# Kernel tuning notes

Hardware: AMD Instinct MI355X
Metric: run time of the kernel (lower is better)

The kernel has to match this reference:

```python
import jax, jax.numpy as jnp
import numpy as np

NUM_HEADS = 8


def setup_inputs() -> dict:
    key = jax.random.key(0)
    ks = jax.random.split(key, 7)
    B, D, N = 16, 512, 2048
    sc = 1.0 / np.sqrt(D)
    return {
        "X_Query": jax.random.normal(ks[0], (B, D, N), jnp.float32),
        "X_Key": jax.random.normal(ks[1], (B, D, N), jnp.float32),
        "X_Value": jax.random.normal(ks[2], (B, D, N), jnp.float32),
        "W_q": jax.random.normal(ks[3], (D, D), jnp.float32) * sc,
        "W_k": jax.random.normal(ks[4], (D, D), jnp.float32) * sc,
        "W_v": jax.random.normal(ks[5], (D, D), jnp.float32) * sc,
        "W_o": jax.random.normal(ks[6], (D, D), jnp.float32) * sc,
    }


def _proj(W, x):
    # Conv1d(D, D, kernel_size=1, bias=False) == channel matmul
    return jnp.einsum('oi,bin->bon', W, x)


def _split_heads(x, h):
    # torch: cat(x.chunk(h, dim=-1), dim=0) -> (h, B, D, N/h) stacked layout
    B, D, N = x.shape
    return x.reshape(B, D, h, N // h).transpose(2, 0, 1, 3)


def _mha(XQ, XK, XV, Wq, Wk, Wv, Wo):
    B, D, N = XQ.shape
    h = NUM_HEADS
    Nh = N // h
    q = _split_heads(_proj(Wq, XQ), h)  # (h, B, D, Nh)
    k = _split_heads(_proj(Wk, XK), h)
    v = _split_heads(_proj(Wv, XV), h)
    # scores over the CHANNEL axis: (h, B, D, D), scaled by sqrt(d_k)=sqrt(Nh)
    scores = jnp.einsum('hbdn,hben->hbde', q, k) / jnp.sqrt(jnp.asarray(Nh, q.dtype))
    p = jax.nn.softmax(scores, axis=-1)
    out = jnp.einsum('hbde,hben->hbdn', p, v)  # (h, B, D, Nh)
    # torch: cat(chunks, dim=0) inverse -> cat along dim=-1
    attn_heads = out.transpose(1, 2, 0, 3).reshape(B, D, N)
    return _proj(Wo, XQ - attn_heads)


def reference(X_Query, X_Key, X_Value, W_q, W_k, W_v, W_o):
    return _mha(X_Query, X_Key, X_Value, W_q, W_k, W_v, W_o)
```

## Files before the change

kernel.cpp:

```cpp
#include <hip/hip_runtime.h>
#include <hip/hip_bf16.h>

#define DD  512
#define NN  2048
#define BB  16
#define NHD 256

typedef unsigned short u16;
typedef __attribute__((ext_vector_type(4))) float f32x4;
typedef __attribute__((ext_vector_type(8))) short s16x8;
typedef __attribute__((ext_vector_type(4))) short s16x4;
typedef __attribute__((ext_vector_type(4))) u16   u16x4;

static __device__ __forceinline__ u16 f2bf(float f) {
  __hip_bfloat16 h = __float2bfloat16(f);
  return *reinterpret_cast<u16*>(&h);
}
static __device__ __forceinline__ float bf2f(u16 u) {
  union { unsigned int i; float f; } v; v.i = ((unsigned int)u) << 16; return v.f;
}
static __device__ __forceinline__ f32x4 mfma_bf16(s16x8 a, s16x8 b, f32x4 c) {
  return __builtin_amdgcn_mfma_f32_16x16x32_bf16(a, b, c, 0, 0, 0);
}
static __device__ __forceinline__ void gload_lds16(const u16* g, u16* l) {
  __builtin_amdgcn_global_load_lds(
      (const __attribute__((address_space(1))) unsigned int*)g,
      (__attribute__((address_space(3))) unsigned int*)l, 16, 0, 0);
}
static __device__ __forceinline__ void barrier_raw() {
  __builtin_amdgcn_sched_barrier(0);
  __builtin_amdgcn_s_barrier();
  __builtin_amdgcn_sched_barrier(0);
}
#define WAITCNT(s) do { asm volatile("s_waitcnt " s ::: "memory"); \
                        __builtin_amdgcn_sched_barrier(0); } while (0)

__global__ __launch_bounds__(256) void k_cvt_w(const float* __restrict__ w0,
                                               const float* __restrict__ w1,
                                               const float* __restrict__ w2,
                                               const float* __restrict__ w3,
                                               u16* __restrict__ out) {
  const float* srcs[4] = {w0, w1, w2, w3};
  const float* s = srcs[blockIdx.y];
  u16* o = out + (size_t)blockIdx.y * (DD * DD);
  int idx = blockIdx.x * 256 + threadIdx.x;
  float4 v = *(const float4*)(s + (size_t)idx * 4);
  u16x4 u = {f2bf(v.x), f2bf(v.y), f2bf(v.z), f2bf(v.w)};
  *(u16x4*)(o + (size_t)idx * 4) = u;
}

template <bool XA>
__global__ __launch_bounds__(256) void k_gemm_proj(
    const float* __restrict__ X, const u16* __restrict__ W,
    u16* __restrict__ C, long long c_bs, int ldc) {
  __shared__ __align__(16) u16 Xb[2][128 * 64];
  __shared__ __align__(16) u16 Wt[2][128 * 64];
  const int tid = threadIdx.x;
  const int lane = tid & 63, w = tid >> 6;
  const int wm = (w >> 1) * 64, wn = (w & 1) * 64;
  const int r = lane & 15, g = lane >> 4;
  f32x4 acc[4][4] = {};

  const int m0 = blockIdx.x * 128, n0 = blockIdx.y * 128, b = blockIdx.z;
  const int xbase = XA ? m0 : n0;
  const int wbase = XA ? n0 : m0;
  const float* Xg = X + (size_t)b * DD * NN + xbase;
  const u16* Wg = W + (size_t)wbase * DD;

  const int nq = tid & 31, ib = (tid >> 5) * 4;
  float4 rv[8];
  auto issue_x = [&](int kt) {
#pragma unroll
    for (int j = 0; j < 2; ++j)
#pragma unroll
      for (int ii = 0; ii < 4; ++ii)
        rv[j * 4 + ii] =
            *(const float4*)(Xg + (size_t)(kt * 64 + j * 32 + ib + ii) * NN + nq * 4);
  };
  auto stage_w = [&](int buf, int kt) {
#pragma unroll
    for (int j2 = 0; j2 < 4; ++j2) {
      int s = j2 * 256 + tid;
      int row = s >> 3, u = s & 7;
      gload_lds16(Wg + (size_t)row * DD + kt * 64 + ((u ^ (row & 7)) * 8),
                  &Wt[buf][s * 8]);
    }
  };
  auto write_x = [&](int buf) {
#pragma unroll
    for (int j = 0; j < 2; ++j) {
      const int k0 = j * 32 + ib;
      const float4 a0 = rv[j*4], a1 = rv[j*4+1], a2 = rv[j*4+2], a3 = rv[j*4+3];
#pragma unroll
      for (int e = 0; e < 4; ++e) {
        const int row = nq * 4 + e;
        float v0, v1, v2, v3;
        if      (e == 0) { v0=a0.x; v1=a1.x; v2=a2.x; v3=a3.x; }
        else if (e == 1) { v0=a0.y; v1=a1.y; v2=a2.y; v3=a3.y; }
        else if (e == 2) { v0=a0.z; v1=a1.z; v2=a2.z; v3=a3.z; }
        else             { v0=a0.w; v1=a1.w; v2=a2.w; v3=a3.w; }
        u16x4 pk = {f2bf(v0), f2bf(v1), f2bf(v2), f2bf(v3)};
        *(u16x4*)((char*)&Xb[buf][0] + row * 128 +
                  (((k0 >> 3) ^ (row & 7)) * 16) + (k0 & 7) * 2) = pk;
      }
    }
  };

  issue_x(0); stage_w(0, 0);
  for (int kt = 0; kt < 8; ++kt) {
    WAITCNT("vmcnt(0)");
    barrier_raw();
    write_x(kt & 1);
    if (kt < 7) { issue_x(kt + 1); stage_w((kt + 1) & 1, kt + 1); }
    WAITCNT("lgkmcnt(0)");
    barrier_raw();
    {
      const u16* Ab_ = XA ? &Xb[kt & 1][0] : &Wt[kt & 1][0];
      const u16* Bb_ = XA ? &Wt[kt & 1][0] : &Xb[kt & 1][0];
#pragma unroll
      for (int ks = 0; ks < 2; ++ks) {
        s16x8 av[4], bv[4];
#pragma unroll
        for (int m = 0; m < 4; ++m) {
          int row = wm + m * 16 + r;
          av[m] = *(const s16x8*)&Ab_[row * 64 + (((ks * 4 + g) ^ (row & 7)) * 8)];
        }
#pragma unroll
        for (int nf = 0; nf < 4; ++nf) {
          int row = wn + nf * 16 + r;
          bv[nf] = *(const s16x8*)&Bb_[row * 64 + (((ks * 4 + g) ^ (row & 7)) * 8)];
        }
#pragma unroll
        for (int m = 0; m < 4; ++m)
#pragma unroll
          for (int nf = 0; nf < 4; ++nf)
            acc[m][nf] = mfma_bf16(av[m], bv[nf], acc[m][nf]);
      }
    }
    WAITCNT("lgkmcnt(0)");
  }

  u16* Cg = C + (size_t)b * c_bs;
#pragma unroll
  for (int m = 0; m < 4; ++m)
#pragma unroll
    for (int nf = 0; nf < 4; ++nf)
#pragma unroll
      for (int j = 0; j < 4; ++j) {
        int row = m0 + wm + m * 16 + g * 4 + j;
        int col = n0 + wn + nf * 16 + r;
        Cg[(size_t)row * ldc + col] = f2bf(acc[m][nf][j]);
      }
}

#define GEMM_STAGE(Ag, lda, Bg, ldb, buf, kt)                                   \
  {                                                                             \
    _Pragma("unroll")                                                           \
    for (int j = 0; j < 4; ++j) {                                               \
      int s = j * 256 + w * 64 + lane;                                          \
      int row = s >> 3, u = s & 7;                                              \
      int col = ((u ^ (row & 7)) * 8);                                          \
      gload_lds16(Ag + (size_t)row * lda + (kt) * 64 + col, &Ab[buf][s * 8]);   \
      gload_lds16(Bg + (size_t)row * ldb + (kt) * 64 + col, &Bb[buf][s * 8]);   \
    }                                                                           \
  }

#define GEMM_COMPUTE(buf)                                                       \
  {                                                                             \
    _Pragma("unroll")                                                           \
    for (int ks = 0; ks < 2; ++ks) {                                            \
      s16x8 av[4], bv[4];                                                       \
      _Pragma("unroll")                                                         \
      for (int m = 0; m < 4; ++m) {                                             \
        int row = wm + m * 16 + r;                                              \
        av[m] = *(const s16x8*)&Ab[buf][row * 64 + (((ks * 4 + g) ^ (row & 7)) * 8)]; \
      }                                                                         \
      _Pragma("unroll")                                                         \
      for (int nf = 0; nf < 4; ++nf) {                                          \
        int row = wn + nf * 16 + r;                                             \
        bv[nf] = *(const s16x8*)&Bb[buf][row * 64 + (((ks * 4 + g) ^ (row & 7)) * 8)]; \
      }                                                                         \
      _Pragma("unroll")                                                         \
      for (int m = 0; m < 4; ++m)                                               \
        _Pragma("unroll")                                                       \
        for (int nf = 0; nf < 4; ++nf)                                          \
          acc[m][nf] = mfma_bf16(av[m], bv[nf], acc[m][nf]);                    \
    }                                                                           \
  }

#define GEMM_PREAMBLE                                                           \
  __shared__ __align__(16) u16 Ab[2][128 * 64];                                 \
  __shared__ __align__(16) u16 Bb[2][128 * 64];                                 \
  const int tid = threadIdx.x;                                                  \
  const int lane = tid & 63, w = tid >> 6;                                      \
  const int wm = (w >> 1) * 64, wn = (w & 1) * 64;                              \
  const int r = lane & 15, g = lane >> 4;                                       \
  f32x4 acc[4][4] = {};

#define GEMM_MAINLOOP(Ag, lda, Bg, ldb, nkt)                                    \
  GEMM_STAGE(Ag, lda, Bg, ldb, 0, 0);                                           \
  __syncthreads();                                                              \
  for (int kt = 0; kt < (nkt) - 1; ++kt) {                                      \
    GEMM_STAGE(Ag, lda, Bg, ldb, (kt & 1) ^ 1, kt + 1);                         \
    GEMM_COMPUTE(kt & 1);                                                       \
    __syncthreads();                                                            \
  }                                                                             \
  GEMM_COMPUTE(((nkt) - 1) & 1);

template <typename OUT_T>
__global__ __launch_bounds__(256) void k_gemm_nt(
    const u16* __restrict__ A, long long a_bs, int lda,
    const u16* __restrict__ B, long long b_bs, int ldb,
    OUT_T* __restrict__ C, long long c_bs, int ldc, int K) {
  GEMM_PREAMBLE
  const int m0 = blockIdx.x * 128, n0 = blockIdx.y * 128;
  const u16* Ag = A + (size_t)blockIdx.z * a_bs + (size_t)m0 * lda;
  const u16* Bg = B + (size_t)blockIdx.z * b_bs + (size_t)n0 * ldb;
  const int nkt = K >> 6;
  GEMM_MAINLOOP(Ag, lda, Bg, ldb, nkt);

  OUT_T* Cg = C + (size_t)blockIdx.z * c_bs;
#pragma unroll
  for (int m = 0; m < 4; ++m)
#pragma unroll
    for (int nf = 0; nf < 4; ++nf)
#pragma unroll
      for (int j = 0; j < 4; ++j) {
        int row = m0 + wm + m * 16 + g * 4 + j;
        int col = n0 + wn + nf * 16 + r;
        float v = acc[m][nf][j];
        if constexpr (sizeof(OUT_T) == 2) Cg[(size_t)row * ldc + col] = f2bf(v);
        else                              Cg[(size_t)row * ldc + col] = v;
      }
}

__global__ __launch_bounds__(512, 4) void k_attn_fused(
    const u16* __restrict__ Qdn, const u16* __restrict__ Kdn,
    const u16* __restrict__ VT,  const float* __restrict__ Xq,
    u16* __restrict__ And) {
  __shared__ __align__(16) u16 L[35072];
  u16* Kr = L;
  u16* Vr = L + 16384;
  u16* Ps = L + 32768;

  const int tid = threadIdx.x;
  const int lane = tid & 63, w = tid >> 6;
  const int r = lane & 15, g = lane >> 4;
  const int dq = w >> 1, eh = w & 1;
  const int nq = w >> 1, dh = w & 1;
  const int bid = blockIdx.x;
  const int dt = bid >> 7, hb = bid & 127;
  const int h = hb & 7, b = hb >> 3;
  const int d0 = dt * 64, hn0 = h * NHD;

  const u16* Qg = Qdn + ((size_t)b * DD + d0) * NN + hn0;
  const u16* Kg = Kdn + ((size_t)b * DD) * NN + hn0;
  const u16* Vg = VT + ((size_t)b * NN + hn0) * DD;

  auto stage_ket = [&](int et) {
    u16* dst = Kr + (et & 1) * 8192;
    const u16* src = Kg + (size_t)(et * 32) * NN;
#pragma unroll
    for (int j = 0; j < 2; ++j) {
      int s = j * 512 + tid;
      int row = s >> 5, u = s & 31;
      gload_lds16(src + (size_t)row * NN + ((u ^ (row & 7)) * 8), dst + s * 8);
    }
  };
  auto stage_vet = [&](int et) {
    u16* dst = Vr + (et & 1) * 8192;
    int rl = tid >> 2, u = tid & 3;
#pragma unroll
    for (int j = 0; j < 2; ++j) {
      int gn = (rl >> 5) * 64 + j * 32 + (rl & 31);
      gload_lds16(Vg + (size_t)gn * DD + et * 32 + ((u ^ (rl & 3)) * 8),
                  dst + j * 4096 + tid * 8);
    }
  };

#pragma unroll
  for (int jj = 0; jj < 4; ++jj) {
    int s = jj * 512 + tid;
    int row = s >> 5, u = s & 31;
    gload_lds16(Qg + (size_t)row * NN + ((u ^ (row & 7)) * 8), L + s * 8);
  }
  WAITCNT("vmcnt(0)");
  barrier_raw();
  s16x8 qf[8];
  {
    const int qrow = dq * 16 + r;
#pragma unroll
    for (int k2 = 0; k2 < 8; ++k2)
      qf[k2] = *(const s16x8*)&L[qrow * 256 + (((k2 * 4 + g) ^ (qrow & 7)) * 8)];
  }
  WAITCNT("lgkmcnt(0)");
  barrier_raw();
  stage_ket(0); stage_vet(0);

  float psum[4] = {};
  f32x4 acc_o[2][2][2] = {};

  for (int et = 0; et < 16; ++et) {
    WAITCNT("vmcnt(2)");
    barrier_raw();
    f32x4 acc_s = {};
    const u16* kb = Kr + (et & 1) * 8192;
    const int rowe = eh * 16 + r;
    __builtin_amdgcn_s_setprio(1);
#pragma unroll
    for (int kq = 0; kq < 8; ++kq) {
      s16x8 bv = *(const s16x8*)&kb[rowe * 256 + (((kq * 4 + g) ^ (rowe & 7)) * 8)];
      acc_s = mfma_bf16(qf[kq], bv, acc_s);
    }
    __builtin_amdgcn_s_setprio(0);
    WAITCNT("lgkmcnt(0)");
    barrier_raw();
    if (et + 1 < 16) { stage_ket(et + 1); stage_vet(et + 1); }
#pragma unroll
    for (int j = 0; j < 4; ++j) {
      int rowd = dq * 16 + g * 4 + j;
      int cole = eh * 16 + r;
      float p = __expf(acc_s[j] * 0.0625f);
      psum[j] += p;
      Ps[rowd * 36 + cole] = f2bf(p);
    }
    WAITCNT("lgkmcnt(0)");
    if (et < 15) WAITCNT("vmcnt(4)");
    else         WAITCNT("vmcnt(0)");
    barrier_raw();
    s16x8 pb[2];
#pragma unroll
    for (int nf = 0; nf < 2; ++nf) {
      int rowd = dh * 32 + nf * 16 + r;
      s16x4 plo = *(const s16x4*)&Ps[rowd * 36 + g * 8];
      s16x4 phi = *(const s16x4*)&Ps[rowd * 36 + g * 8 + 4];
      pb[nf] = __builtin_shufflevector(plo, phi, 0, 1, 2, 3, 4, 5, 6, 7);
    }
    __builtin_amdgcn_s_setprio(1);
#pragma unroll
    for (int j = 0; j < 2; ++j) {
      const u16* vb = Vr + (et & 1) * 8192 + j * 4096;
#pragma unroll
      for (int ms = 0; ms < 2; ++ms) {
        int rl = nq * 32 + ms * 16 + r;
        s16x8 av = *(const s16x8*)((const char*)vb + rl * 64 + ((g * 16) ^ ((rl & 3) << 4)));
        acc_o[j][ms][0] = mfma_bf16(av, pb[0], acc_o[j][ms][0]);
        acc_o[j][ms][1] = mfma_bf16(av, pb[1], acc_o[j][ms][1]);
      }
    }
    __builtin_amdgcn_s_setprio(0);
    WAITCNT("lgkmcnt(0)");
  }

  barrier_raw();
  float* rs = (float*)L;
#pragma unroll
  for (int j = 0; j < 4; ++j) {
    float v = psum[j];
    v += __shfl_xor(v, 1);
    v += __shfl_xor(v, 2);
    v += __shfl_xor(v, 4);
    v += __shfl_xor(v, 8);
    if (r == 0) rs[w * 16 + g * 4 + j] = v;
  }
  __syncthreads();
  if (tid < 64) {
    int dqi = tid >> 4, i = tid & 15;
    rs[128 + tid] = 1.0f / (rs[(dqi * 2) * 16 + i] + rs[(dqi * 2 + 1) * 16 + i]);
  }
  __syncthreads();

  const float* Xqf = Xq + ((size_t)b * DD + d0) * NN + hn0;
  u16* Ag = And + ((size_t)b * NN + hn0) * DD + d0;
#pragma unroll
  for (int j = 0; j < 2; ++j)
#pragma unroll
    for (int ms = 0; ms < 2; ++ms)
#pragma unroll
      for (int nf = 0; nf < 2; ++nf) {
        const int dc = dh * 32 + nf * 16 + r;
        const float inv = rs[128 + dc];
#pragma unroll
        for (int jj = 0; jj < 4; ++jj) {
          const int npos = nq * 64 + j * 32 + ms * 16 + g * 4 + jj;
          float o = acc_o[j][ms][nf][jj] * inv;
          float xq = Xqf[(size_t)dc * NN + npos];
          Ag[(size_t)npos * DD + dc] = f2bf(xq - o);
        }
      }
}

extern "C" void kernel_launch(void* const* d_in, const int* in_sizes, int n_in,
                              void* d_out, int out_size, void* d_ws, size_t ws_size,
                              hipStream_t stream) {
  const float* Xq = (const float*)d_in[0];
  const float* Xk = (const float*)d_in[1];
  const float* Xv = (const float*)d_in[2];
  const float* Wq = (const float*)d_in[3];
  const float* Wk = (const float*)d_in[4];
  const float* Wv = (const float*)d_in[5];
  const float* Wo = (const float*)d_in[6];
  float* out = (float*)d_out;

  char* ws = (char*)d_ws;
  const size_t MB = 1024 * 1024;
  u16* Wb  = (u16*)ws;
  u16* Qdn = (u16*)(ws + 2 * MB);
  u16* And = (u16*)(ws + 34 * MB);
  u16* VTb = (u16*)d_out;
  u16* Kdn = (u16*)d_out + (size_t)BB * NN * DD;

  k_cvt_w<<<dim3(256, 4), 256, 0, stream>>>(Wq, Wk, Wv, Wo, Wb);

  k_gemm_proj<false><<<dim3(DD / 128, NN / 128, BB), 256, 0, stream>>>(
      Xq, Wb, Qdn, (long long)DD * NN, NN);
  k_gemm_proj<false><<<dim3(DD / 128, NN / 128, BB), 256, 0, stream>>>(
      Xk, Wb + DD * DD, Kdn, (long long)DD * NN, NN);
  k_gemm_proj<true><<<dim3(NN / 128, DD / 128, BB), 256, 0, stream>>>(
      Xv, Wb + 2 * DD * DD, VTb, (long long)NN * DD, DD);

  k_attn_fused<<<dim3(1024), 512, 0, stream>>>(Qdn, Kdn, VTb, Xq, And);

  k_gemm_nt<float><<<dim3(DD / 128, NN / 128, BB), 256, 0, stream>>>(
      Wb + 3 * DD * DD, 0, DD,
      And, (long long)NN * DD, DD,
      out, (long long)DD * NN, NN, DD);
}
```

Baseline: 256.5 us.

## Read projection weights directly from global memory and stage Xq tile through LDS

The projection GEMM stops staging weight tiles into shared memory. MFMA operands for the weights now come straight from global memory (expected to hit in L2/L1), and the X tile uses a single LDS buffer with a reworked transpose-write pattern. This frees LDS and removes the W staging loads, but it drops double buffering and adds a barrier per k-step. Separately, the attention epilogue first loads the Xq tile into LDS with coalesced float4 loads, so the residual subtraction no longer does strided scalar global reads.

```diff
diff --git a/kernel.cpp b/kernel.cpp
--- a/kernel.cpp
+++ b/kernel.cpp
@@ -53,8 +53,7 @@
 __global__ __launch_bounds__(256) void k_gemm_proj(
     const float* __restrict__ X, const u16* __restrict__ W,
     u16* __restrict__ C, long long c_bs, int ldc) {
-  __shared__ __align__(16) u16 Xb[2][128 * 64];
-  __shared__ __align__(16) u16 Wt[2][128 * 64];
+  __shared__ __align__(16) u16 Xb[128 * 64];
   const int tid = threadIdx.x;
   const int lane = tid & 63, w = tid >> 6;
   const int wm = (w >> 1) * 64, wn = (w & 1) * 64;
@@ -62,82 +61,63 @@
   f32x4 acc[4][4] = {};
 
   const int m0 = blockIdx.x * 128, n0 = blockIdx.y * 128, b = blockIdx.z;
-  const int xbase = XA ? m0 : n0;
-  const int wbase = XA ? n0 : m0;
-  const float* Xg = X + (size_t)b * DD * NN + xbase;
-  const u16* Wg = W + (size_t)wbase * DD;
-
-  const int nq = tid & 31, ib = (tid >> 5) * 4;
+  const int nb = XA ? m0 : n0;
+  const int wb = XA ? n0 : m0;
+  const float* Xg = X + (size_t)b * DD * NN + nb;
+  const u16* Wg = W + (size_t)wb * DD;
+
+  const int n4 = (tid & 31) * 4;
+  const int k8 = (tid >> 5) * 8;
   float4 rv[8];
   auto issue_x = [&](int kt) {
 #pragma unroll
-    for (int j = 0; j < 2; ++j)
-#pragma unroll
-      for (int ii = 0; ii < 4; ++ii)
-        rv[j * 4 + ii] =
-            *(const float4*)(Xg + (size_t)(kt * 64 + j * 32 + ib + ii) * NN + nq * 4);
+    for (int kk = 0; kk < 8; ++kk)
+      rv[kk] = *(const float4*)(Xg + (size_t)(kt * 64 + k8 + kk) * NN + n4);
   };
-  auto stage_w = [&](int buf, int kt) {
-#pragma unroll
-    for (int j2 = 0; j2 < 4; ++j2) {
-      int s = j2 * 256 + tid;
-      int row = s >> 3, u = s & 7;
-      gload_lds16(Wg + (size_t)row * DD + kt * 64 + ((u ^ (row & 7)) * 8),
-                  &Wt[buf][s * 8]);
+  auto write_x = [&]() {
+#pragma unroll
+    for (int e = 0; e < 4; ++e) {
+      const int row = n4 + e;
+      const int base = row * 128 + (((k8 >> 3) ^ (row & 7)) * 16);
+#pragma unroll
+      for (int kb = 0; kb < 2; ++kb) {
+        u16x4 pk = {f2bf(rv[kb * 4 + 0][e]), f2bf(rv[kb * 4 + 1][e]),
+                    f2bf(rv[kb * 4 + 2][e]), f2bf(rv[kb * 4 + 3][e])};
+        *(u16x4*)((char*)Xb + base + kb * 8) = pk;
+      }
     }
   };
-  auto write_x = [&](int buf) {
-#pragma unroll
-    for (int j = 0; j < 2; ++j) {
-      const int k0 = j * 32 + ib;
-      const float4 a0 = rv[j*4], a1 = rv[j*4+1], a2 = rv[j*4+2], a3 = rv[j*4+3];
-#pragma unroll
-      for (int e = 0; e < 4; ++e) {
-        const int row = nq * 4 + e;
-        float v0, v1, v2, v3;
-        if      (e == 0) { v0=a0.x; v1=a1.x; v2=a2.x; v3=a3.x; }
-        else if (e == 1) { v0=a0.y; v1=a1.y; v2=a2.y; v3=a3.y; }
-        else if (e == 2) { v0=a0.z; v1=a1.z; v2=a2.z; v3=a3.z; }
-        else             { v0=a0.w; v1=a1.w; v2=a2.w; v3=a3.w; }
-        u16x4 pk = {f2bf(v0), f2bf(v1), f2bf(v2), f2bf(v3)};
-        *(u16x4*)((char*)&Xb[buf][0] + row * 128 +
-                  (((k0 >> 3) ^ (row & 7)) * 16) + (k0 & 7) * 2) = pk;
-      }
-    }
-  };
-
-  issue_x(0); stage_w(0, 0);
+
+  issue_x(0);
   for (int kt = 0; kt < 8; ++kt) {
     WAITCNT("vmcnt(0)");
-    barrier_raw();
-    write_x(kt & 1);
-    if (kt < 7) { issue_x(kt + 1); stage_w((kt + 1) & 1, kt + 1); }
+    write_x();
+    if (kt < 7) issue_x(kt + 1);
     WAITCNT("lgkmcnt(0)");
     barrier_raw();
-    {
-      const u16* Ab_ = XA ? &Xb[kt & 1][0] : &Wt[kt & 1][0];
-      const u16* Bb_ = XA ? &Wt[kt & 1][0] : &Xb[kt & 1][0];
-#pragma unroll
-      for (int ks = 0; ks < 2; ++ks) {
-        s16x8 av[4], bv[4];
-#pragma unroll
-        for (int m = 0; m < 4; ++m) {
-          int row = wm + m * 16 + r;
-          av[m] = *(const s16x8*)&Ab_[row * 64 + (((ks * 4 + g) ^ (row & 7)) * 8)];
-        }
-#pragma unroll
-        for (int nf = 0; nf < 4; ++nf) {
-          int row = wn + nf * 16 + r;
-          bv[nf] = *(const s16x8*)&Bb_[row * 64 + (((ks * 4 + g) ^ (row & 7)) * 8)];
-        }
-#pragma unroll
-        for (int m = 0; m < 4; ++m)
-#pragma unroll
-          for (int nf = 0; nf < 4; ++nf)
-            acc[m][nf] = mfma_bf16(av[m], bv[nf], acc[m][nf]);
-      }
+#pragma unroll
+    for (int ks = 0; ks < 2; ++ks) {
+      s16x8 wv[4], xv[4];
+#pragma unroll
+      for (int m = 0; m < 4; ++m) {
+        int wrow = (XA ? wn : wm) + m * 16 + r;
+        wv[m] = *(const s16x8*)(Wg + (size_t)wrow * DD + kt * 64 + (ks * 4 + g) * 8);
+      }
+#pragma unroll
+      for (int m = 0; m < 4; ++m) {
+        int xrow = (XA ? wm : wn) + m * 16 + r;
+        xv[m] = *(const s16x8*)((char*)Xb + xrow * 128 +
+                                (((ks * 4 + g) ^ (xrow & 7)) * 16));
+      }
+#pragma unroll
+      for (int m = 0; m < 4; ++m)
+#pragma unroll
+        for (int nf = 0; nf < 4; ++nf)
+          acc[m][nf] = XA ? mfma_bf16(xv[m], wv[nf], acc[m][nf])
+                          : mfma_bf16(wv[m], xv[nf], acc[m][nf]);
     }
     WAITCNT("lgkmcnt(0)");
+    barrier_raw();
   }
 
   u16* Cg = C + (size_t)b * c_bs;
@@ -369,8 +349,21 @@
     rs[128 + tid] = 1.0f / (rs[(dqi * 2) * 16 + i] + rs[(dqi * 2 + 1) * 16 + i]);
   }
   __syncthreads();
-
-  const float* Xqf = Xq + ((size_t)b * DD + d0) * NN + hn0;
+  const float inv0 = rs[128 + dh * 32 + r];
+  const float inv1 = rs[128 + dh * 32 + 16 + r];
+  __syncthreads();
+
+  float* Lf = (float*)L;
+  const float* XqF = Xq + ((size_t)b * DD + d0) * NN + hn0;
+#pragma unroll
+  for (int jj = 0; jj < 8; ++jj) {
+    int s = jj * 512 + tid;
+    int row = s >> 6, slot = s & 63;
+    f32x4 v = *(const f32x4*)(XqF + (size_t)row * NN + slot * 4);
+    *(f32x4*)&Lf[row * 260 + slot * 4] = v;
+  }
+  __syncthreads();
+
   u16* Ag = And + ((size_t)b * NN + hn0) * DD + d0;
 #pragma unroll
   for (int j = 0; j < 2; ++j)
@@ -379,12 +372,12 @@
 #pragma unroll
       for (int nf = 0; nf < 2; ++nf) {
         const int dc = dh * 32 + nf * 16 + r;
-        const float inv = rs[128 + dc];
+        const float inv = nf ? inv1 : inv0;
 #pragma unroll
         for (int jj = 0; jj < 4; ++jj) {
           const int npos = nq * 64 + j * 32 + ms * 16 + g * 4 + jj;
           float o = acc_o[j][ms][nf][jj] * inv;
-          float xq = Xqf[(size_t)dc * NN + npos];
+          float xq = Lf[dc * 260 + npos];
           Ag[(size_t)npos * DD + dc] = f2bf(xq - o);
         }
       }
```

Result: slower. 316.6 us (+23.5%).
